# Performance work log

Measured on AMD Instinct MI355X. Metric: run time of the kernel, lower is better.

## Reference

```python
import jax, jax.numpy as jnp
import numpy as np

HEADS = 4
DIM_HEAD = 32
GROUPS = 32  # min(256//4, 32)
EPS = 1e-5


def setup_inputs() -> dict:
    key = jax.random.key(0)
    ks = jax.random.split(key, 6)
    B, C, H, W = 16, 256, 64, 64
    hidden = HEADS * DIM_HEAD  # 128
    return {
        "x": jax.random.normal(ks[0], (B, C, H, W), dtype=jnp.float32),
        "gn_w": jax.random.uniform(ks[1], (C,), dtype=jnp.float32),
        "gn_b": jax.random.normal(ks[2], (C,), dtype=jnp.float32) * 0.05,
        "qkv_w": jax.random.normal(ks[3], (3 * hidden, C), dtype=jnp.float32) * 0.05,
        "qkv_b": jax.random.normal(ks[4], (3 * hidden,), dtype=jnp.float32) * 0.05,
        "out_w": jax.random.normal(ks[5], (C, hidden), dtype=jnp.float32) * 0.05,
        "out_b": jnp.zeros((C,), dtype=jnp.float32),
    }


def _forward_single(x, gn_w, gn_b, qkv_w, qkv_b, out_w, out_b):
    # x: (c, h, w)
    c, h, w = x.shape
    # GroupNorm over (channels-in-group, h, w)
    xg = x.reshape(GROUPS, c // GROUPS, h, w)
    mean = xg.mean(axis=(1, 2, 3), keepdims=True)
    var = xg.var(axis=(1, 2, 3), keepdims=True)
    xn = ((xg - mean) * jax.lax.rsqrt(var + EPS)).reshape(c, h, w)
    xn = xn * gn_w[:, None, None] + gn_b[:, None, None]
    # 1x1 conv QKV projection
    qkv = jnp.einsum('oc,chw->ohw', qkv_w, xn) + qkv_b[:, None, None]
    qkv = qkv.reshape(3, HEADS, DIM_HEAD, h * w)
    q, k, v = qkv[0], qkv[1], qkv[2]
    k = jax.nn.softmax(k, axis=-1)  # softmax over spatial
    context = jnp.einsum('hdn,hen->hde', k, v)   # (heads, d, d)
    out = jnp.einsum('hde,hdn->hen', context, q)  # (heads, d, n)
    out = out.reshape(HEADS * DIM_HEAD, h, w)
    # 1x1 conv output projection
    return jnp.einsum('oc,chw->ohw', out_w, out) + out_b[:, None, None]


def reference(x, gn_w, gn_b, qkv_w, qkv_b, out_w, out_b):
    f = lambda xi: _forward_single(xi, gn_w, gn_b, qkv_w, qkv_b, out_w, out_b)
    return jax.vmap(f)(x)
```

## Files before the change

### kernel.cpp

```cpp
#include <hip/hip_runtime.h>
#include <stdint.h>

typedef unsigned short u16;
typedef __attribute__((ext_vector_type(8))) short bf16x8;
typedef __attribute__((ext_vector_type(4))) float f32x4;

#define B_   16
#define C_   256
#define HW_  4096
#define QR_  384
#define HID_ 128

__device__ __forceinline__ float b2f(u16 u) {
  union { uint32_t i; float f; } v; v.i = ((uint32_t)u) << 16; return v.f;
}
__device__ __forceinline__ u16 f2b(float f) {
  union { float f; uint32_t i; } v; v.f = f;
  uint32_t r = (v.i + 0x7FFFu + ((v.i >> 16) & 1u)) >> 16;
  return (u16)r;
}

__global__ __launch_bounds__(256) void gn_stats_conv_kernel(
    const float* __restrict__ x, const float* __restrict__ gnw,
    const float* __restrict__ gnb, float* __restrict__ scale,
    float* __restrict__ shiftv,
    const float* __restrict__ qkvw, u16* __restrict__ cqkvw)
{
  if (blockIdx.x >= 512) {
    int i = (blockIdx.x - 512) * 256 + threadIdx.x;
    float4 f = ((const float4*)qkvw)[i];
    ushort4 o;
    o.x = f2b(f.x); o.y = f2b(f.y); o.z = f2b(f.z); o.w = f2b(f.w);
    ((ushort4*)cqkvw)[i] = o;
    return;
  }
  int b = blockIdx.x >> 5, g = blockIdx.x & 31;
  const float* p = x + ((size_t)b * C_ + g * 8) * HW_;
  int t = threadIdx.x;
  float s = 0.f, sq = 0.f;
#pragma unroll
  for (int i = 0; i < 16; ++i) {
    float4 u0 = *(const float4*)(p + t * 8 + i * 2048);
    float4 u1 = *(const float4*)(p + t * 8 + i * 2048 + 4);
    s  += u0.x + u0.y + u0.z + u0.w + u1.x + u1.y + u1.z + u1.w;
    sq += u0.x*u0.x + u0.y*u0.y + u0.z*u0.z + u0.w*u0.w
        + u1.x*u1.x + u1.y*u1.y + u1.z*u1.z + u1.w*u1.w;
  }
#pragma unroll
  for (int off = 32; off > 0; off >>= 1) {
    s  += __shfl_down(s, off);
    sq += __shfl_down(sq, off);
  }
  __shared__ float ps[4], pq[4], mr[2];
  int lane = t & 63, w = t >> 6;
  if (lane == 0) { ps[w] = s; pq[w] = sq; }
  __syncthreads();
  if (t == 0) {
    float S = ps[0] + ps[1] + ps[2] + ps[3];
    float Q = pq[0] + pq[1] + pq[2] + pq[3];
    float mean = S * (1.f / 32768.f);
    float var  = Q * (1.f / 32768.f) - mean * mean;
    mr[0] = mean; mr[1] = rsqrtf(var + 1e-5f);
  }
  __syncthreads();
  if (t < 8) {
    int c = g * 8 + t;
    float sc = gnw[c] * mr[1];
    scale[b * C_ + c]  = sc;
    shiftv[b * C_ + c] = gnb[c] - mr[0] * sc;
  }
}

__global__ __launch_bounds__(256) void gn_transpose_kernel(
    const float* __restrict__ x, u16* __restrict__ dst,
    const float* __restrict__ scale, const float* __restrict__ shiftv)
{
  int nt = blockIdx.x, ct = blockIdx.y, b = blockIdx.z;
  const float* S = x + (size_t)b * C_ * HW_;
  u16* D = dst + (size_t)b * HW_ * C_;
  __shared__ __align__(16) u16 tile[64][136];
  int t = threadIdx.x;
  int n0 = nt * 128, c0 = ct * 64;
  int r = t >> 2, seg = (t & 3) * 32;
  float sc = scale[(size_t)b * C_ + c0 + r];
  float sh = shiftv[(size_t)b * C_ + c0 + r];
#pragma unroll
  for (int i = 0; i < 4; ++i) {
    const float* rp = S + (size_t)(c0 + r) * HW_ + n0 + seg + i * 8;
    float4 u0 = *(const float4*)(rp);
    float4 u1 = *(const float4*)(rp + 4);
    float f[8] = {u0.x, u0.y, u0.z, u0.w, u1.x, u1.y, u1.z, u1.w};
    uint4 o;
    uint32_t* op = (uint32_t*)&o;
#pragma unroll
    for (int j = 0; j < 4; ++j) {
      op[j] = (uint32_t)f2b(f[2 * j] * sc + sh)
            | ((uint32_t)f2b(f[2 * j + 1] * sc + sh) << 16);
    }
    *(uint4*)&tile[r][seg + i * 8] = o;
  }
  __syncthreads();
#pragma unroll
  for (int i = 0; i < 4; ++i) {
    int m = t * 4 + i;
    int n_l = m >> 3, cg = (m & 7) * 8;
    union { u16 v[8]; uint4 q; } pk;
#pragma unroll
    for (int e = 0; e < 8; ++e) pk.v[e] = tile[cg + e][n_l];
    *(uint4*)(D + (size_t)(n0 + n_l) * C_ + c0 + cg) = pk.q;
  }
}

__global__ __launch_bounds__(256) void qkv_gemm_kernel(
    const u16* __restrict__ A, const u16* __restrict__ Bt,
    const float* __restrict__ bias, u16* __restrict__ qkv,
    u16* __restrict__ q_t)
{
  const int K = C_;
  int nt = blockIdx.x, mt = blockIdx.y, b = blockIdx.z;
  const u16* Ab = A + (size_t)mt * 128 * K;
  const u16* Bb = Bt + (size_t)b * HW_ * C_ + (size_t)nt * 128 * K;
  __shared__ __align__(16) u16 smem[128 * 136];
  u16* lA = smem;
  u16* lB = smem + 8192;
  int t = threadIdx.x;
  int lane = t & 63, w = t >> 6;
  int quad = lane >> 4, l16 = lane & 15;
  int wm = (w >> 1) * 64, wn = (w & 1) * 64;
  f32x4 acc[4][4];
#pragma unroll
  for (int i = 0; i < 4; ++i)
#pragma unroll
    for (int j = 0; j < 4; ++j)
#pragma unroll
      for (int r = 0; r < 4; ++r) acc[i][j][r] = 0.f;

  for (int k0 = 0; k0 < K; k0 += 64) {
    __syncthreads();
#pragma unroll
    for (int q = 0; q < 4; ++q) {
      int ch = q * 256 + t;
      int row = ch >> 3, off = (ch & 7) * 8;
      __builtin_amdgcn_global_load_lds(
          (const __attribute__((address_space(1))) void*)(Ab + (size_t)row * K + k0 + off),
          (__attribute__((address_space(3))) void*)(lA + ch * 8), 16, 0, 0);
      __builtin_amdgcn_global_load_lds(
          (const __attribute__((address_space(1))) void*)(Bb + (size_t)row * K + k0 + off),
          (__attribute__((address_space(3))) void*)(lB + ch * 8), 16, 0, 0);
    }
    __syncthreads();
    const bf16x8* A8 = (const bf16x8*)lA;
    const bf16x8* B8 = (const bf16x8*)lB;
#pragma unroll
    for (int kk = 0; kk < 2; ++kk) {
      bf16x8 af[4], bfr[4];
#pragma unroll
      for (int i = 0; i < 4; ++i) af[i]  = A8[(wm + i * 16 + l16) * 8 + kk * 4 + quad];
#pragma unroll
      for (int j = 0; j < 4; ++j) bfr[j] = B8[(wn + j * 16 + l16) * 8 + kk * 4 + quad];
#pragma unroll
      for (int i = 0; i < 4; ++i)
#pragma unroll
        for (int j = 0; j < 4; ++j)
          acc[i][j] = __builtin_amdgcn_mfma_f32_16x16x32_bf16(af[i], bfr[j],
                                                              acc[i][j], 0, 0, 0);
    }
  }

  if (mt == 0) {
    __syncthreads();
#pragma unroll
    for (int i = 0; i < 4; ++i) {
      int o0 = wm + i * 16 + quad * 4;
      float b0 = bias[o0], b1 = bias[o0 + 1], b2 = bias[o0 + 2], b3 = bias[o0 + 3];
#pragma unroll
      for (int j = 0; j < 4; ++j) {
        int n_l = wn + j * 16 + l16;
        uint2 pk;
        pk.x = (uint32_t)f2b(acc[i][j][0] + b0) | ((uint32_t)f2b(acc[i][j][1] + b1) << 16);
        pk.y = (uint32_t)f2b(acc[i][j][2] + b2) | ((uint32_t)f2b(acc[i][j][3] + b3) << 16);
        *(uint2*)&smem[n_l * 136 + o0] = pk;
      }
    }
    __syncthreads();
    int n_l = t >> 1, half = t & 1;
    u16* dst = q_t + (size_t)b * HW_ * HID_ + (size_t)(nt * 128 + n_l) * HID_ + half * 64;
    const u16* srcp = smem + n_l * 136 + half * 64;
#pragma unroll
    for (int i = 0; i < 8; ++i)
      *(uint4*)(dst + i * 8) = *(const uint4*)(srcp + i * 8);
  } else {
#pragma unroll
    for (int i = 0; i < 4; ++i) {
#pragma unroll
      for (int rg = 0; rg < 4; ++rg) {
        int o = mt * 128 + wm + i * 16 + quad * 4 + rg;
        float bsv = bias[o];
        size_t rowbase = (size_t)b * QR_ * HW_ + (size_t)o * HW_;
#pragma unroll
        for (int j = 0; j < 4; ++j) {
          int n = nt * 128 + wn + j * 16 + l16;
          qkv[rowbase + n] = f2b(acc[i][j][rg] + bsv);
        }
      }
    }
  }
}

__global__ __launch_bounds__(1024) void ctxwf_kernel(
    const u16* __restrict__ qkv, const float* __restrict__ outw,
    u16* __restrict__ wf)
{
  int b = blockIdx.x >> 2, h = blockIdx.x & 3;
  const u16* kb = qkv + ((size_t)b * QR_ + 128 + h * 32) * HW_;
  const u16* vb = qkv + ((size_t)b * QR_ + 256 + h * 32) * HW_;
  int t = threadIdx.x;
  int w = t >> 6, lane = t & 63;
  int quad = lane >> 4, l16 = lane & 15;
  __shared__ float part[16][1024];
  __shared__ float cs[1024];
  __shared__ float2 sred[1024];
  __shared__ float sinv[32];
  f32x4 acc[2][2];
#pragma unroll
  for (int i = 0; i < 2; ++i)
#pragma unroll
    for (int j = 0; j < 2; ++j)
#pragma unroll
      for (int r = 0; r < 4; ++r) acc[i][j][r] = 0.f;
  float s0 = 0.f, s1 = 0.f;
  int kbase = w * 256;
  for (int it = 0; it < 8; ++it) {
    int n0 = kbase + it * 32 + quad * 8;
    bf16x8 k0 = *(const bf16x8*)(kb + (size_t)l16 * HW_ + n0);
    bf16x8 k1 = *(const bf16x8*)(kb + (size_t)(16 + l16) * HW_ + n0);
    bf16x8 v0 = *(const bf16x8*)(vb + (size_t)l16 * HW_ + n0);
    bf16x8 v1 = *(const bf16x8*)(vb + (size_t)(16 + l16) * HW_ + n0);
    bf16x8 a0, a1;
    const u16* k0p = (const u16*)&k0; u16* a0p = (u16*)&a0;
    const u16* k1p = (const u16*)&k1; u16* a1p = (u16*)&a1;
#pragma unroll
    for (int e = 0; e < 8; ++e) {
      float e0 = __expf(b2f(k0p[e]));
      float e1 = __expf(b2f(k1p[e]));
      s0 += e0; s1 += e1;
      a0p[e] = f2b(e0);
      a1p[e] = f2b(e1);
    }
    acc[0][0] = __builtin_amdgcn_mfma_f32_16x16x32_bf16(a0, v0, acc[0][0], 0, 0, 0);
    acc[0][1] = __builtin_amdgcn_mfma_f32_16x16x32_bf16(a0, v1, acc[0][1], 0, 0, 0);
    acc[1][0] = __builtin_amdgcn_mfma_f32_16x16x32_bf16(a1, v0, acc[1][0], 0, 0, 0);
    acc[1][1] = __builtin_amdgcn_mfma_f32_16x16x32_bf16(a1, v1, acc[1][1], 0, 0, 0);
  }
#pragma unroll
  for (int i = 0; i < 2; ++i)
#pragma unroll
    for (int j = 0; j < 2; ++j)
#pragma unroll
      for (int r = 0; r < 4; ++r) {
        int d = i * 16 + quad * 4 + r;
        int e = j * 16 + l16;
        part[w][d * 32 + e] = acc[i][j][r];
      }
  sred[t] = make_float2(s0, s1);
  __syncthreads();
  {
    float a = 0.f;
#pragma unroll
    for (int ww = 0; ww < 16; ++ww) a += part[ww][t];
    cs[t] = a;
  }
  if (t < 32) {
    int d = t, lsel = d & 15;
    float ssum = 0.f;
#pragma unroll
    for (int ww = 0; ww < 16; ++ww)
#pragma unroll
      for (int q = 0; q < 4; ++q) {
        float2 v2 = sred[ww * 64 + q * 16 + lsel];
        ssum += (d < 16) ? v2.x : v2.y;
      }
    sinv[d] = 1.f / ssum;
  }
  __syncthreads();

  int o = t & 255, dg = t >> 8;
  const float* wr = outw + (size_t)o * HID_ + h * 32;
  float wv[32];
#pragma unroll
  for (int e = 0; e < 32; ++e) wv[e] = wr[e];
  union { u16 v[8]; uint4 q; } pk;
#pragma unroll
  for (int dd = 0; dd < 8; ++dd) {
    int d = dg * 8 + dd;
    float a = 0.f;
#pragma unroll
    for (int e = 0; e < 32; ++e) a += wv[e] * cs[d * 32 + e];
    pk.v[dd] = f2b(a * sinv[d]);
  }
  *(uint4*)(wf + ((size_t)b * C_ + o) * HID_ + h * 32 + dg * 8) = pk.q;
}

__global__ __launch_bounds__(256) void out_gemm_kernel(
    const u16* __restrict__ A, const u16* __restrict__ Bt,
    const float* __restrict__ bias, float* __restrict__ Cout)
{
  const int K = HID_;
  int nt = blockIdx.x, mt = blockIdx.y, b = blockIdx.z;
  const u16* Ab = A + (size_t)b * C_ * HID_ + (size_t)mt * 128 * K;
  const u16* Bb = Bt + (size_t)b * HW_ * HID_ + (size_t)nt * 128 * K;
  __shared__ __align__(16) u16 lA[128 * 64];
  __shared__ __align__(16) u16 lB[128 * 64];
  int t = threadIdx.x;
  int lane = t & 63, w = t >> 6;
  int quad = lane >> 4, l16 = lane & 15;
  int wm = (w >> 1) * 64, wn = (w & 1) * 64;
  f32x4 acc[4][4];
#pragma unroll
  for (int i = 0; i < 4; ++i)
#pragma unroll
    for (int j = 0; j < 4; ++j)
#pragma unroll
      for (int r = 0; r < 4; ++r) acc[i][j][r] = 0.f;

  for (int k0 = 0; k0 < K; k0 += 64) {
    __syncthreads();
#pragma unroll
    for (int q = 0; q < 4; ++q) {
      int ch = q * 256 + t;
      int row = ch >> 3, off = (ch & 7) * 8;
      __builtin_amdgcn_global_load_lds(
          (const __attribute__((address_space(1))) void*)(Ab + (size_t)row * K + k0 + off),
          (__attribute__((address_space(3))) void*)(lA + ch * 8), 16, 0, 0);
      __builtin_amdgcn_global_load_lds(
          (const __attribute__((address_space(1))) void*)(Bb + (size_t)row * K + k0 + off),
          (__attribute__((address_space(3))) void*)(lB + ch * 8), 16, 0, 0);
    }
    __syncthreads();
    const bf16x8* A8 = (const bf16x8*)lA;
    const bf16x8* B8 = (const bf16x8*)lB;
#pragma unroll
    for (int kk = 0; kk < 2; ++kk) {
      bf16x8 af[4], bfr[4];
#pragma unroll
      for (int i = 0; i < 4; ++i) af[i]  = A8[(wm + i * 16 + l16) * 8 + kk * 4 + quad];
#pragma unroll
      for (int j = 0; j < 4; ++j) bfr[j] = B8[(wn + j * 16 + l16) * 8 + kk * 4 + quad];
#pragma unroll
      for (int i = 0; i < 4; ++i)
#pragma unroll
        for (int j = 0; j < 4; ++j)
          acc[i][j] = __builtin_amdgcn_mfma_f32_16x16x32_bf16(af[i], bfr[j],
                                                              acc[i][j], 0, 0, 0);
    }
  }
#pragma unroll
  for (int i = 0; i < 4; ++i) {
#pragma unroll
    for (int rg = 0; rg < 4; ++rg) {
      int o = mt * 128 + wm + i * 16 + quad * 4 + rg;
      float bsv = bias[o];
      size_t rowbase = (size_t)b * C_ * HW_ + (size_t)o * HW_;
#pragma unroll
      for (int j = 0; j < 4; ++j) {
        int n = nt * 128 + wn + j * 16 + l16;
        Cout[rowbase + n] = acc[i][j][rg] + bsv;
      }
    }
  }
}

extern "C" void kernel_launch(void* const* d_in, const int* in_sizes, int n_in,
                              void* d_out, int out_size, void* d_ws, size_t ws_size,
                              hipStream_t stream)
{
  const float* x    = (const float*)d_in[0];
  const float* gnw  = (const float*)d_in[1];
  const float* gnb  = (const float*)d_in[2];
  const float* qkvw = (const float*)d_in[3];
  const float* qkvb = (const float*)d_in[4];
  const float* outw = (const float*)d_in[5];
  const float* outb = (const float*)d_in[6];

  char* p = (char*)d_ws;
  float* scale  = (float*)p;            p += (size_t)B_ * C_ * 4;
  float* shiftv = (float*)p;            p += (size_t)B_ * C_ * 4;
  u16* cqkvw = (u16*)p;                 p += (size_t)QR_ * C_ * 2;
  u16* xn_t  = (u16*)p;                 p += (size_t)B_ * HW_ * C_ * 2;
  u16* qkv   = (u16*)p;                 p += (size_t)B_ * QR_ * HW_ * 2;
  u16* q_t   = (u16*)p;                 p += (size_t)B_ * HW_ * HID_ * 2;
  u16* wf    = (u16*)p;

  gn_stats_conv_kernel<<<608, 256, 0, stream>>>(x, gnw, gnb, scale, shiftv,
                                                qkvw, cqkvw);
  gn_transpose_kernel<<<dim3(32, 4, 16), 256, 0, stream>>>(x, xn_t, scale, shiftv);
  qkv_gemm_kernel<<<dim3(32, 3, 16), 256, 0, stream>>>(cqkvw, xn_t, qkvb, qkv, q_t);
  ctxwf_kernel<<<64, 1024, 0, stream>>>(qkv, outw, wf);
  out_gemm_kernel<<<dim3(32, 2, 16), 256, 0, stream>>>(wf, q_t, outb, (float*)d_out);
}
```

Measured before the change: 205.8 us.

## Fuse all stages into one persistent kernel with grid barriers

Replaces the five-kernel pipeline with a single persistent kernel of 256 blocks of 512 threads. The stages (GroupNorm stats, normalize-transpose, QKV GEMM, context, output GEMM) are separated by software grid barriers built on atomics. The context reduction is spread over all blocks with atomicAdd into global buffers, replacing the old 64-block kernel. The folded output weight is recomputed per tile inside the output GEMM. This removes launch gaps and the under-parallelised ctx stage, at the cost of spin-barrier overhead, a co-residency requirement for all 256 blocks, and redundant per-tile weight folding.

After: 449.4 us. +118.3%, slower.

```diff
diff --git a/kernel.cpp b/kernel.cpp
--- a/kernel.cpp
+++ b/kernel.cpp
@@ -8,8 +8,8 @@
 #define B_   16
 #define C_   256
 #define HW_  4096
-#define QR_  384
 #define HID_ 128
+#define NBLK 256
 
 __device__ __forceinline__ float b2f(u16 u) {
   union { uint32_t i; float f; } v; v.i = ((uint32_t)u) << 16; return v.f;
@@ -20,351 +20,397 @@
   return (u16)r;
 }
 
-__global__ __launch_bounds__(256) void gn_stats_conv_kernel(
+__global__ void init_kernel(unsigned* bar) {
+  if (threadIdx.x < 8) bar[threadIdx.x] = 0u;
+}
+
+__device__ __forceinline__ void grid_barrier(unsigned* bar) {
+  __syncthreads();
+  if (threadIdx.x == 0) {
+    __threadfence();
+    unsigned g = __hip_atomic_load(&bar[1], __ATOMIC_RELAXED, __HIP_MEMORY_SCOPE_AGENT);
+    unsigned a = __hip_atomic_fetch_add(&bar[0], 1u, __ATOMIC_ACQ_REL, __HIP_MEMORY_SCOPE_AGENT);
+    if (a == NBLK - 1) {
+      __hip_atomic_store(&bar[0], 0u, __ATOMIC_RELAXED, __HIP_MEMORY_SCOPE_AGENT);
+      __hip_atomic_store(&bar[1], g + 1u, __ATOMIC_RELEASE, __HIP_MEMORY_SCOPE_AGENT);
+    } else {
+      while (__hip_atomic_load(&bar[1], __ATOMIC_ACQUIRE, __HIP_MEMORY_SCOPE_AGENT) == g) {
+        __builtin_amdgcn_s_sleep(1);
+      }
+    }
+  }
+  __syncthreads();
+}
+
+__global__ __launch_bounds__(512, 2) void mega_kernel(
     const float* __restrict__ x, const float* __restrict__ gnw,
-    const float* __restrict__ gnb, float* __restrict__ scale,
-    float* __restrict__ shiftv,
-    const float* __restrict__ qkvw, u16* __restrict__ cqkvw)
+    const float* __restrict__ gnb, const float* __restrict__ qkvw,
+    const float* __restrict__ qkvb, const float* __restrict__ outw,
+    const float* __restrict__ outb, float* __restrict__ out,
+    unsigned* bar, float* scale, float* shiftv, u16* cqkvw,
+    u16* xn_t, u16* kv, u16* q_t, float* ctxg, float* sbuf)
 {
-  if (blockIdx.x >= 512) {
-    int i = (blockIdx.x - 512) * 256 + threadIdx.x;
-    float4 f = ((const float4*)qkvw)[i];
-    ushort4 o;
-    o.x = f2b(f.x); o.y = f2b(f.y); o.z = f2b(f.z); o.w = f2b(f.w);
-    ((ushort4*)cqkvw)[i] = o;
-    return;
-  }
-  int b = blockIdx.x >> 5, g = blockIdx.x & 31;
-  const float* p = x + ((size_t)b * C_ + g * 8) * HW_;
+  __shared__ __align__(16) char smem_raw[119296];
   int t = threadIdx.x;
-  float s = 0.f, sq = 0.f;
-#pragma unroll
-  for (int i = 0; i < 16; ++i) {
-    float4 u0 = *(const float4*)(p + t * 8 + i * 2048);
-    float4 u1 = *(const float4*)(p + t * 8 + i * 2048 + 4);
-    s  += u0.x + u0.y + u0.z + u0.w + u1.x + u1.y + u1.z + u1.w;
-    sq += u0.x*u0.x + u0.y*u0.y + u0.z*u0.z + u0.w*u0.w
-        + u1.x*u1.x + u1.y*u1.y + u1.z*u1.z + u1.w*u1.w;
-  }
-#pragma unroll
-  for (int off = 32; off > 0; off >>= 1) {
-    s  += __shfl_down(s, off);
-    sq += __shfl_down(sq, off);
-  }
-  __shared__ float ps[4], pq[4], mr[2];
-  int lane = t & 63, w = t >> 6;
-  if (lane == 0) { ps[w] = s; pq[w] = sq; }
-  __syncthreads();
-  if (t == 0) {
-    float S = ps[0] + ps[1] + ps[2] + ps[3];
-    float Q = pq[0] + pq[1] + pq[2] + pq[3];
-    float mean = S * (1.f / 32768.f);
-    float var  = Q * (1.f / 32768.f) - mean * mean;
-    mr[0] = mean; mr[1] = rsqrtf(var + 1e-5f);
-  }
-  __syncthreads();
-  if (t < 8) {
-    int c = g * 8 + t;
-    float sc = gnw[c] * mr[1];
-    scale[b * C_ + c]  = sc;
-    shiftv[b * C_ + c] = gnb[c] - mr[0] * sc;
-  }
-}
-
-__global__ __launch_bounds__(256) void gn_transpose_kernel(
-    const float* __restrict__ x, u16* __restrict__ dst,
-    const float* __restrict__ scale, const float* __restrict__ shiftv)
-{
-  int nt = blockIdx.x, ct = blockIdx.y, b = blockIdx.z;
-  const float* S = x + (size_t)b * C_ * HW_;
-  u16* D = dst + (size_t)b * HW_ * C_;
-  __shared__ __align__(16) u16 tile[64][136];
-  int t = threadIdx.x;
-  int n0 = nt * 128, c0 = ct * 64;
-  int r = t >> 2, seg = (t & 3) * 32;
-  float sc = scale[(size_t)b * C_ + c0 + r];
-  float sh = shiftv[(size_t)b * C_ + c0 + r];
-#pragma unroll
-  for (int i = 0; i < 4; ++i) {
-    const float* rp = S + (size_t)(c0 + r) * HW_ + n0 + seg + i * 8;
-    float4 u0 = *(const float4*)(rp);
-    float4 u1 = *(const float4*)(rp + 4);
-    float f[8] = {u0.x, u0.y, u0.z, u0.w, u1.x, u1.y, u1.z, u1.w};
-    uint4 o;
-    uint32_t* op = (uint32_t*)&o;
-#pragma unroll
-    for (int j = 0; j < 4; ++j) {
-      op[j] = (uint32_t)f2b(f[2 * j] * sc + sh)
-            | ((uint32_t)f2b(f[2 * j + 1] * sc + sh) << 16);
-    }
-    *(uint4*)&tile[r][seg + i * 8] = o;
-  }
-  __syncthreads();
-#pragma unroll
-  for (int i = 0; i < 4; ++i) {
-    int m = t * 4 + i;
-    int n_l = m >> 3, cg = (m & 7) * 8;
-    union { u16 v[8]; uint4 q; } pk;
-#pragma unroll
-    for (int e = 0; e < 8; ++e) pk.v[e] = tile[cg + e][n_l];
-    *(uint4*)(D + (size_t)(n0 + n_l) * C_ + c0 + cg) = pk.q;
-  }
-}
-
-__global__ __launch_bounds__(256) void qkv_gemm_kernel(
-    const u16* __restrict__ A, const u16* __restrict__ Bt,
-    const float* __restrict__ bias, u16* __restrict__ qkv,
-    u16* __restrict__ q_t)
-{
-  const int K = C_;
-  int nt = blockIdx.x, mt = blockIdx.y, b = blockIdx.z;
-  const u16* Ab = A + (size_t)mt * 128 * K;
-  const u16* Bb = Bt + (size_t)b * HW_ * C_ + (size_t)nt * 128 * K;
-  __shared__ __align__(16) u16 smem[128 * 136];
-  u16* lA = smem;
-  u16* lB = smem + 8192;
-  int t = threadIdx.x;
-  int lane = t & 63, w = t >> 6;
-  int quad = lane >> 4, l16 = lane & 15;
-  int wm = (w >> 1) * 64, wn = (w & 1) * 64;
-  f32x4 acc[4][4];
-#pragma unroll
-  for (int i = 0; i < 4; ++i)
-#pragma unroll
-    for (int j = 0; j < 4; ++j)
-#pragma unroll
-      for (int r = 0; r < 4; ++r) acc[i][j][r] = 0.f;
-
-  for (int k0 = 0; k0 < K; k0 += 64) {
+  int blk = blockIdx.x;
+
+  {
+    int gid = blk * 512 + t;
+    if (gid < 24576) {
+      float4 f = ((const float4*)qkvw)[gid];
+      ushort4 o;
+      o.x = f2b(f.x); o.y = f2b(f.y); o.z = f2b(f.z); o.w = f2b(f.w);
+      ((ushort4*)cqkvw)[gid] = o;
+    } else if (gid < 24576 + 16896) {
+      ((float4*)ctxg)[gid - 24576] = make_float4(0.f, 0.f, 0.f, 0.f);
+    }
+    int half = t >> 8, tid = t & 255;
+    int grp = blk * 2 + half;
+    int b = grp >> 5, g = grp & 31;
+    const float* p = x + ((size_t)b * C_ + g * 8) * HW_;
+    float s = 0.f, sq = 0.f;
+#pragma unroll
+    for (int i = 0; i < 16; ++i) {
+      float4 u0 = *(const float4*)(p + tid * 8 + i * 2048);
+      float4 u1 = *(const float4*)(p + tid * 8 + i * 2048 + 4);
+      s  += u0.x + u0.y + u0.z + u0.w + u1.x + u1.y + u1.z + u1.w;
+      sq += u0.x*u0.x + u0.y*u0.y + u0.z*u0.z + u0.w*u0.w
+          + u1.x*u1.x + u1.y*u1.y + u1.z*u1.z + u1.w*u1.w;
+    }
+#pragma unroll
+    for (int off = 32; off > 0; off >>= 1) {
+      s  += __shfl_down(s, off);
+      sq += __shfl_down(sq, off);
+    }
+    float* ps = (float*)smem_raw;
+    float* pq = ps + 8;
+    float* mrA = pq + 8;
+    int lane = t & 63, w = t >> 6;
+    if (lane == 0) { ps[w] = s; pq[w] = sq; }
     __syncthreads();
-#pragma unroll
-    for (int q = 0; q < 4; ++q) {
-      int ch = q * 256 + t;
-      int row = ch >> 3, off = (ch & 7) * 8;
-      __builtin_amdgcn_global_load_lds(
-          (const __attribute__((address_space(1))) void*)(Ab + (size_t)row * K + k0 + off),
-          (__attribute__((address_space(3))) void*)(lA + ch * 8), 16, 0, 0);
-      __builtin_amdgcn_global_load_lds(
-          (const __attribute__((address_space(1))) void*)(Bb + (size_t)row * K + k0 + off),
-          (__attribute__((address_space(3))) void*)(lB + ch * 8), 16, 0, 0);
+    if (tid == 0) {
+      float S = ps[half*4] + ps[half*4+1] + ps[half*4+2] + ps[half*4+3];
+      float Q = pq[half*4] + pq[half*4+1] + pq[half*4+2] + pq[half*4+3];
+      float mean = S * (1.f / 32768.f);
+      float var  = Q * (1.f / 32768.f) - mean * mean;
+      mrA[half*2]   = mean;
+      mrA[half*2+1] = rsqrtf(var + 1e-5f);
     }
     __syncthreads();
-    const bf16x8* A8 = (const bf16x8*)lA;
-    const bf16x8* B8 = (const bf16x8*)lB;
-#pragma unroll
-    for (int kk = 0; kk < 2; ++kk) {
-      bf16x8 af[4], bfr[4];
-#pragma unroll
-      for (int i = 0; i < 4; ++i) af[i]  = A8[(wm + i * 16 + l16) * 8 + kk * 4 + quad];
-#pragma unroll
-      for (int j = 0; j < 4; ++j) bfr[j] = B8[(wn + j * 16 + l16) * 8 + kk * 4 + quad];
+    if (tid < 8) {
+      int c = g * 8 + tid;
+      float sc = gnw[c] * mrA[half*2+1];
+      scale[b * C_ + c]  = sc;
+      shiftv[b * C_ + c] = gnb[c] - mrA[half*2] * sc;
+    }
+  }
+  grid_barrier(bar);
+
+  {
+    int sg = t >> 8, tid = t & 255;
+#pragma unroll 1
+    for (int iter = 0; iter < 4; ++iter) {
+      int task = iter * 512 + blk * 2 + sg;
+      int nt = task & 31, ct = (task >> 5) & 3, b = task >> 7;
+      const float* S = x + (size_t)b * C_ * HW_;
+      u16* D = xn_t + (size_t)b * HW_ * C_;
+      u16* tl = (u16*)smem_raw + sg * 8704;
+      int n0 = nt * 128, c0 = ct * 64;
+      int r = tid >> 2, seg = (tid & 3) * 32;
+      float sc = scale[(size_t)b * C_ + c0 + r];
+      float sh = shiftv[(size_t)b * C_ + c0 + r];
+#pragma unroll
+      for (int i = 0; i < 4; ++i) {
+        const float* rp = S + (size_t)(c0 + r) * HW_ + n0 + seg + i * 8;
+        float4 u0 = *(const float4*)(rp);
+        float4 u1 = *(const float4*)(rp + 4);
+        float f[8] = {u0.x, u0.y, u0.z, u0.w, u1.x, u1.y, u1.z, u1.w};
+        uint4 o;
+        uint32_t* op = (uint32_t*)&o;
+#pragma unroll
+        for (int j = 0; j < 4; ++j)
+          op[j] = (uint32_t)f2b(f[2*j] * sc + sh)
+                | ((uint32_t)f2b(f[2*j+1] * sc + sh) << 16);
+        *(uint4*)&tl[r * 136 + seg + i * 8] = o;
+      }
+      __syncthreads();
+#pragma unroll
+      for (int i = 0; i < 4; ++i) {
+        int m = tid * 4 + i;
+        int n_l = m >> 3, cg = (m & 7) * 8;
+        union { u16 v[8]; uint4 q; } pk;
+#pragma unroll
+        for (int e = 0; e < 8; ++e) pk.v[e] = tl[(cg + e) * 136 + n_l];
+        *(uint4*)(D + (size_t)(n0 + n_l) * C_ + c0 + cg) = pk.q;
+      }
+      __syncthreads();
+    }
+  }
+  grid_barrier(bar);
+
+  {
+    u16* lA = (u16*)smem_raw;
+    u16* lB = lA + 8192;
+    int lane = t & 63, w = t >> 6;
+    int quad = lane >> 4, l16 = lane & 15;
+    int wm = (w >> 2) * 64, wn = (w & 3) * 64;
+#pragma unroll 1
+    for (int iter = 0; iter < 3; ++iter) {
+      int task = iter * 256 + blk;
+      int b = task / 48, r48 = task % 48;
+      int mt = r48 >> 4, nt = r48 & 15;
+      const u16* Ab = cqkvw + (size_t)mt * 128 * 256;
+      const u16* Bb = xn_t + (size_t)b * HW_ * C_ + (size_t)nt * 256 * 256;
+      f32x4 acc[4][4];
 #pragma unroll
       for (int i = 0; i < 4; ++i)
 #pragma unroll
         for (int j = 0; j < 4; ++j)
-          acc[i][j] = __builtin_amdgcn_mfma_f32_16x16x32_bf16(af[i], bfr[j],
-                                                              acc[i][j], 0, 0, 0);
-    }
-  }
-
-  if (mt == 0) {
+#pragma unroll
+          for (int r = 0; r < 4; ++r) acc[i][j][r] = 0.f;
+      for (int k0 = 0; k0 < 256; k0 += 64) {
+        __syncthreads();
+#pragma unroll
+        for (int q = 0; q < 6; ++q) {
+          int ch = q * 512 + t;
+          if (ch < 1024) {
+            int row = ch >> 3, off = (ch & 7) * 8;
+            __builtin_amdgcn_global_load_lds(
+                (const __attribute__((address_space(1))) void*)(Ab + (size_t)row * 256 + k0 + off),
+                (__attribute__((address_space(3))) void*)(lA + ch * 8), 16, 0, 0);
+          } else {
+            int c2 = ch - 1024;
+            int row = c2 >> 3, off = (c2 & 7) * 8;
+            __builtin_amdgcn_global_load_lds(
+                (const __attribute__((address_space(1))) void*)(Bb + (size_t)row * 256 + k0 + off),
+                (__attribute__((address_space(3))) void*)(lB + c2 * 8), 16, 0, 0);
+          }
+        }
+        __syncthreads();
+        const bf16x8* A8 = (const bf16x8*)lA;
+        const bf16x8* B8 = (const bf16x8*)lB;
+#pragma unroll
+        for (int kk = 0; kk < 2; ++kk) {
+          bf16x8 af[4], bfr[4];
+#pragma unroll
+          for (int i = 0; i < 4; ++i) af[i]  = A8[(wm + i * 16 + l16) * 8 + kk * 4 + quad];
+#pragma unroll
+          for (int j = 0; j < 4; ++j) bfr[j] = B8[(wn + j * 16 + l16) * 8 + kk * 4 + quad];
+#pragma unroll
+          for (int i = 0; i < 4; ++i)
+#pragma unroll
+            for (int j = 0; j < 4; ++j)
+              acc[i][j] = __builtin_amdgcn_mfma_f32_16x16x32_bf16(af[i], bfr[j],
+                                                                  acc[i][j], 0, 0, 0);
+        }
+      }
+      __syncthreads();
+      if (mt == 0) {
+        u16* ot = (u16*)smem_raw;
+#pragma unroll
+        for (int i = 0; i < 4; ++i) {
+          int o0 = wm + i * 16 + quad * 4;
+          float b0 = qkvb[o0], b1 = qkvb[o0+1], b2 = qkvb[o0+2], b3 = qkvb[o0+3];
+#pragma unroll
+          for (int j = 0; j < 4; ++j) {
+            int n_l = wn + j * 16 + l16;
+            uint2 pk;
+            pk.x = (uint32_t)f2b(acc[i][j][0] + b0) | ((uint32_t)f2b(acc[i][j][1] + b1) << 16);
+            pk.y = (uint32_t)f2b(acc[i][j][2] + b2) | ((uint32_t)f2b(acc[i][j][3] + b3) << 16);
+            *(uint2*)&ot[n_l * 136 + o0] = pk;
+          }
+        }
+      } else {
+#pragma unroll
+        for (int i = 0; i < 4; ++i) {
+#pragma unroll
+          for (int rg = 0; rg < 4; ++rg) {
+            int o = mt * 128 + wm + i * 16 + quad * 4 + rg;
+            float bsv = qkvb[o];
+            u16* kr = kv + ((size_t)b * 256 + (o - 128)) * HW_;
+#pragma unroll
+            for (int j = 0; j < 4; ++j) {
+              int n = nt * 256 + wn + j * 16 + l16;
+              kr[n] = f2b(acc[i][j][rg] + bsv);
+            }
+          }
+        }
+      }
+      __syncthreads();
+      if (mt == 0) {
+        int n_l = t >> 1, half = t & 1;
+        u16* dst = q_t + (size_t)b * HW_ * HID_ + (size_t)(nt * 256 + n_l) * HID_ + half * 64;
+        const u16* sp = (const u16*)smem_raw + n_l * 136 + half * 64;
+#pragma unroll
+        for (int i = 0; i < 8; ++i)
+          *(uint4*)(dst + i * 8) = *(const uint4*)(sp + i * 8);
+      }
+    }
+  }
+  grid_barrier(bar);
+
+  {
+    int sg = t >> 8, tid = t & 255;
+    int task = blk * 2 + sg;
+    int b = task >> 5, h = (task >> 3) & 3, chunk = task & 7;
+    const u16* kb = kv + ((size_t)b * 256 + h * 32) * HW_;
+    const u16* vb = kv + ((size_t)b * 256 + 128 + h * 32) * HW_;
+    int wl = tid >> 6, lane = t & 63;
+    int quad = lane >> 4, l16 = lane & 15;
+    float* part = (float*)smem_raw + sg * 4608;
+    float* sred = part + 4096;
+    f32x4 acc[2][2];
+#pragma unroll
+    for (int i = 0; i < 2; ++i)
+#pragma unroll
+      for (int j = 0; j < 2; ++j)
+#pragma unroll
+        for (int r = 0; r < 4; ++r) acc[i][j][r] = 0.f;
+    float s0 = 0.f, s1 = 0.f;
+    int base = chunk * 512 + wl * 128;
+#pragma unroll 1
+    for (int it = 0; it < 4; ++it) {
+      int n0 = base + it * 32 + quad * 8;
+      bf16x8 k0 = *(const bf16x8*)(kb + (size_t)l16 * HW_ + n0);
+      bf16x8 k1 = *(const bf16x8*)(kb + (size_t)(16 + l16) * HW_ + n0);
+      bf16x8 v0 = *(const bf16x8*)(vb + (size_t)l16 * HW_ + n0);
+      bf16x8 v1 = *(const bf16x8*)(vb + (size_t)(16 + l16) * HW_ + n0);
+      bf16x8 a0, a1;
+      const u16* k0p = (const u16*)&k0; u16* a0p = (u16*)&a0;
+      const u16* k1p = (const u16*)&k1; u16* a1p = (u16*)&a1;
+#pragma unroll
+      for (int e = 0; e < 8; ++e) {
+        float e0 = __expf(b2f(k0p[e]));
+        float e1 = __expf(b2f(k1p[e]));
+        s0 += e0; s1 += e1;
+        a0p[e] = f2b(e0); a1p[e] = f2b(e1);
+      }
+      acc[0][0] = __builtin_amdgcn_mfma_f32_16x16x32_bf16(a0, v0, acc[0][0], 0, 0, 0);
+      acc[0][1] = __builtin_amdgcn_mfma_f32_16x16x32_bf16(a0, v1, acc[0][1], 0, 0, 0);
+      acc[1][0] = __builtin_amdgcn_mfma_f32_16x16x32_bf16(a1, v0, acc[1][0], 0, 0, 0);
+      acc[1][1] = __builtin_amdgcn_mfma_f32_16x16x32_bf16(a1, v1, acc[1][1], 0, 0, 0);
+    }
+#pragma unroll
+    for (int i = 0; i < 2; ++i)
+#pragma unroll
+      for (int j = 0; j < 2; ++j)
+#pragma unroll
+        for (int r = 0; r < 4; ++r) {
+          int d = i * 16 + quad * 4 + r;
+          int e = j * 16 + l16;
+          part[wl * 1024 + d * 32 + e] = acc[i][j][r];
+        }
+    sred[wl * 128 + (lane & 63) * 2]     = s0;
+    sred[wl * 128 + (lane & 63) * 2 + 1] = s1;
     __syncthreads();
+    float* cb = ctxg + (size_t)(b * 4 + h) * 1024;
 #pragma unroll
     for (int i = 0; i < 4; ++i) {
-      int o0 = wm + i * 16 + quad * 4;
-      float b0 = bias[o0], b1 = bias[o0 + 1], b2 = bias[o0 + 2], b3 = bias[o0 + 3];
-#pragma unroll
-      for (int j = 0; j < 4; ++j) {
-        int n_l = wn + j * 16 + l16;
-        uint2 pk;
-        pk.x = (uint32_t)f2b(acc[i][j][0] + b0) | ((uint32_t)f2b(acc[i][j][1] + b1) << 16);
-        pk.y = (uint32_t)f2b(acc[i][j][2] + b2) | ((uint32_t)f2b(acc[i][j][3] + b3) << 16);
-        *(uint2*)&smem[n_l * 136 + o0] = pk;
-      }
-    }
-    __syncthreads();
-    int n_l = t >> 1, half = t & 1;
-    u16* dst = q_t + (size_t)b * HW_ * HID_ + (size_t)(nt * 128 + n_l) * HID_ + half * 64;
-    const u16* srcp = smem + n_l * 136 + half * 64;
-#pragma unroll
-    for (int i = 0; i < 8; ++i)
-      *(uint4*)(dst + i * 8) = *(const uint4*)(srcp + i * 8);
-  } else {
-#pragma unroll
-    for (int i = 0; i < 4; ++i) {
-#pragma unroll
-      for (int rg = 0; rg < 4; ++rg) {
-        int o = mt * 128 + wm + i * 16 + quad * 4 + rg;
-        float bsv = bias[o];
-        size_t rowbase = (size_t)b * QR_ * HW_ + (size_t)o * HW_;
-#pragma unroll
-        for (int j = 0; j < 4; ++j) {
-          int n = nt * 128 + wn + j * 16 + l16;
-          qkv[rowbase + n] = f2b(acc[i][j][rg] + bsv);
-        }
-      }
-    }
-  }
-}
-
-__global__ __launch_bounds__(1024) void ctxwf_kernel(
-    const u16* __restrict__ qkv, const float* __restrict__ outw,
-    u16* __restrict__ wf)
-{
-  int b = blockIdx.x >> 2, h = blockIdx.x & 3;
-  const u16* kb = qkv + ((size_t)b * QR_ + 128 + h * 32) * HW_;
-  const u16* vb = qkv + ((size_t)b * QR_ + 256 + h * 32) * HW_;
-  int t = threadIdx.x;
-  int w = t >> 6, lane = t & 63;
-  int quad = lane >> 4, l16 = lane & 15;
-  __shared__ float part[16][1024];
-  __shared__ float cs[1024];
-  __shared__ float2 sred[1024];
-  __shared__ float sinv[32];
-  f32x4 acc[2][2];
-#pragma unroll
-  for (int i = 0; i < 2; ++i)
-#pragma unroll
-    for (int j = 0; j < 2; ++j)
-#pragma unroll
-      for (int r = 0; r < 4; ++r) acc[i][j][r] = 0.f;
-  float s0 = 0.f, s1 = 0.f;
-  int kbase = w * 256;
-  for (int it = 0; it < 8; ++it) {
-    int n0 = kbase + it * 32 + quad * 8;
-    bf16x8 k0 = *(const bf16x8*)(kb + (size_t)l16 * HW_ + n0);
-    bf16x8 k1 = *(const bf16x8*)(kb + (size_t)(16 + l16) * HW_ + n0);
-    bf16x8 v0 = *(const bf16x8*)(vb + (size_t)l16 * HW_ + n0);
-    bf16x8 v1 = *(const bf16x8*)(vb + (size_t)(16 + l16) * HW_ + n0);
-    bf16x8 a0, a1;
-    const u16* k0p = (const u16*)&k0; u16* a0p = (u16*)&a0;
-    const u16* k1p = (const u16*)&k1; u16* a1p = (u16*)&a1;
-#pragma unroll
-    for (int e = 0; e < 8; ++e) {
-      float e0 = __expf(b2f(k0p[e]));
-      float e1 = __expf(b2f(k1p[e]));
-      s0 += e0; s1 += e1;
-      a0p[e] = f2b(e0);
-      a1p[e] = f2b(e1);
-    }
-    acc[0][0] = __builtin_amdgcn_mfma_f32_16x16x32_bf16(a0, v0, acc[0][0], 0, 0, 0);
-    acc[0][1] = __builtin_amdgcn_mfma_f32_16x16x32_bf16(a0, v1, acc[0][1], 0, 0, 0);
-    acc[1][0] = __builtin_amdgcn_mfma_f32_16x16x32_bf16(a1, v0, acc[1][0], 0, 0, 0);
-    acc[1][1] = __builtin_amdgcn_mfma_f32_16x16x32_bf16(a1, v1, acc[1][1], 0, 0, 0);
-  }
-#pragma unroll
-  for (int i = 0; i < 2; ++i)
-#pragma unroll
-    for (int j = 0; j < 2; ++j)
-#pragma unroll
-      for (int r = 0; r < 4; ++r) {
-        int d = i * 16 + quad * 4 + r;
-        int e = j * 16 + l16;
-        part[w][d * 32 + e] = acc[i][j][r];
-      }
-  sred[t] = make_float2(s0, s1);
-  __syncthreads();
+      int idx = tid + i * 256;
+      atomicAdd(&cb[idx], part[idx] + part[1024 + idx] + part[2048 + idx] + part[3072 + idx]);
+    }
+    if (tid < 32) {
+      int d = tid;
+      float ss = 0.f;
+#pragma unroll
+      for (int w2 = 0; w2 < 4; ++w2)
+#pragma unroll
+        for (int q = 0; q < 4; ++q)
+          ss += sred[w2 * 128 + (q * 16 + (d & 15)) * 2 + (d >> 4)];
+      atomicAdd(&sbuf[(b * 4 + h) * 32 + d], ss);
+    }
+  }
+  grid_barrier(bar);
+
   {
-    float a = 0.f;
-#pragma unroll
-    for (int ww = 0; ww < 16; ++ww) a += part[ww][t];
-    cs[t] = a;
-  }
-  if (t < 32) {
-    int d = t, lsel = d & 15;
-    float ssum = 0.f;
-#pragma unroll
-    for (int ww = 0; ww < 16; ++ww)
+    u16* wfA = (u16*)smem_raw;
+    u16* lB  = (u16*)smem_raw + 256 * 136;
+    float* ctxs = (float*)(smem_raw + 69632 + 32768);
+    float* sinv = (float*)(smem_raw + 69632 + 32768 + 16384);
+    int lane = t & 63, w = t >> 6;
+    int quad = lane >> 4, l16 = lane & 15;
+    int wm = (w >> 1) * 64, wn = (w & 1) * 64;
+#pragma unroll 1
+    for (int iter = 0; iter < 2; ++iter) {
+      int task = iter * 256 + blk;
+      int nt = task & 31, b = task >> 5;
+      __syncthreads();
+      {
+        const float* cb = ctxg + (size_t)b * 4096;
+#pragma unroll
+        for (int i = 0; i < 8; ++i) ctxs[t + i * 512] = cb[t + i * 512];
+        if (t < 128) sinv[t] = 1.f / sbuf[b * 128 + t];
+      }
 #pragma unroll
       for (int q = 0; q < 4; ++q) {
-        float2 v2 = sred[ww * 64 + q * 16 + lsel];
-        ssum += (d < 16) ? v2.x : v2.y;
-      }
-    sinv[d] = 1.f / ssum;
-  }
-  __syncthreads();
-
-  int o = t & 255, dg = t >> 8;
-  const float* wr = outw + (size_t)o * HID_ + h * 32;
-  float wv[32];
-#pragma unroll
-  for (int e = 0; e < 32; ++e) wv[e] = wr[e];
-  union { u16 v[8]; uint4 q; } pk;
-#pragma unroll
-  for (int dd = 0; dd < 8; ++dd) {
-    int d = dg * 8 + dd;
-    float a = 0.f;
-#pragma unroll
-    for (int e = 0; e < 32; ++e) a += wv[e] * cs[d * 32 + e];
-    pk.v[dd] = f2b(a * sinv[d]);
-  }
-  *(uint4*)(wf + ((size_t)b * C_ + o) * HID_ + h * 32 + dg * 8) = pk.q;
-}
-
-__global__ __launch_bounds__(256) void out_gemm_kernel(
-    const u16* __restrict__ A, const u16* __restrict__ Bt,
-    const float* __restrict__ bias, float* __restrict__ Cout)
-{
-  const int K = HID_;
-  int nt = blockIdx.x, mt = blockIdx.y, b = blockIdx.z;
-  const u16* Ab = A + (size_t)b * C_ * HID_ + (size_t)mt * 128 * K;
-  const u16* Bb = Bt + (size_t)b * HW_ * HID_ + (size_t)nt * 128 * K;
-  __shared__ __align__(16) u16 lA[128 * 64];
-  __shared__ __align__(16) u16 lB[128 * 64];
-  int t = threadIdx.x;
-  int lane = t & 63, w = t >> 6;
-  int quad = lane >> 4, l16 = lane & 15;
-  int wm = (w >> 1) * 64, wn = (w & 1) * 64;
-  f32x4 acc[4][4];
-#pragma unroll
-  for (int i = 0; i < 4; ++i)
-#pragma unroll
-    for (int j = 0; j < 4; ++j)
-#pragma unroll
-      for (int r = 0; r < 4; ++r) acc[i][j][r] = 0.f;
-
-  for (int k0 = 0; k0 < K; k0 += 64) {
-    __syncthreads();
-#pragma unroll
-    for (int q = 0; q < 4; ++q) {
-      int ch = q * 256 + t;
-      int row = ch >> 3, off = (ch & 7) * 8;
-      __builtin_amdgcn_global_load_lds(
-          (const __attribute__((address_space(1))) void*)(Ab + (size_t)row * K + k0 + off),
-          (__attribute__((address_space(3))) void*)(lA + ch * 8), 16, 0, 0);
-      __builtin_amdgcn_global_load_lds(
-          (const __attribute__((address_space(1))) void*)(Bb + (size_t)row * K + k0 + off),
-          (__attribute__((address_space(3))) void*)(lB + ch * 8), 16, 0, 0);
-    }
-    __syncthreads();
-    const bf16x8* A8 = (const bf16x8*)lA;
-    const bf16x8* B8 = (const bf16x8*)lB;
-#pragma unroll
-    for (int kk = 0; kk < 2; ++kk) {
-      bf16x8 af[4], bfr[4];
-#pragma unroll
-      for (int i = 0; i < 4; ++i) af[i]  = A8[(wm + i * 16 + l16) * 8 + kk * 4 + quad];
-#pragma unroll
-      for (int j = 0; j < 4; ++j) bfr[j] = B8[(wn + j * 16 + l16) * 8 + kk * 4 + quad];
+        int ch = q * 512 + t;
+        int row = ch >> 4, off = (ch & 15) * 8;
+        __builtin_amdgcn_global_load_lds(
+            (const __attribute__((address_space(1))) void*)(q_t + ((size_t)b * HW_ + nt * 128 + row) * HID_ + off),
+            (__attribute__((address_space(3))) void*)(lB + ch * 8), 16, 0, 0);
+      }
+      __syncthreads();
+      {
+        int o = t >> 1, half = t & 1;
+        const float* wr = outw + (size_t)o * HID_ + half * 64;
+        float wv[64];
+#pragma unroll
+        for (int e = 0; e < 64; ++e) wv[e] = wr[e];
+        u16* dr = wfA + o * 136 + half * 64;
+#pragma unroll
+        for (int hh = 0; hh < 2; ++hh) {
+          int h = half * 2 + hh;
+#pragma unroll
+          for (int d = 0; d < 32; d += 2) {
+            float a0 = 0.f, a1 = 0.f;
+#pragma unroll
+            for (int e = 0; e < 32; ++e) {
+              a0 += wv[hh * 32 + e] * ctxs[h * 1024 + d * 32 + e];
+              a1 += wv[hh * 32 + e] * ctxs[h * 1024 + (d + 1) * 32 + e];
+            }
+            a0 *= sinv[half * 64 + hh * 32 + d];
+            a1 *= sinv[half * 64 + hh * 32 + d + 1];
+            *(uint32_t*)&dr[hh * 32 + d] = (uint32_t)f2b(a0) | ((uint32_t)f2b(a1) << 16);
+          }
+        }
+      }
+      __syncthreads();
+      f32x4 acc[4][4];
 #pragma unroll
       for (int i = 0; i < 4; ++i)
 #pragma unroll
         for (int j = 0; j < 4; ++j)
-          acc[i][j] = __builtin_amdgcn_mfma_f32_16x16x32_bf16(af[i], bfr[j],
-                                                              acc[i][j], 0, 0, 0);
-    }
-  }
-#pragma unroll
-  for (int i = 0; i < 4; ++i) {
-#pragma unroll
-    for (int rg = 0; rg < 4; ++rg) {
-      int o = mt * 128 + wm + i * 16 + quad * 4 + rg;
-      float bsv = bias[o];
-      size_t rowbase = (size_t)b * C_ * HW_ + (size_t)o * HW_;
-#pragma unroll
-      for (int j = 0; j < 4; ++j) {
-        int n = nt * 128 + wn + j * 16 + l16;
-        Cout[rowbase + n] = acc[i][j][rg] + bsv;
+#pragma unroll
+          for (int r = 0; r < 4; ++r) acc[i][j][r] = 0.f;
+      const bf16x8* A8 = (const bf16x8*)wfA;
+      const bf16x8* B8 = (const bf16x8*)lB;
+#pragma unroll
+      for (int kk = 0; kk < 4; ++kk) {
+        bf16x8 af[4], bfr[4];
+#pragma unroll
+        for (int i = 0; i < 4; ++i) af[i]  = A8[(wm + i * 16 + l16) * 17 + kk * 4 + quad];
+#pragma unroll
+        for (int j = 0; j < 4; ++j) bfr[j] = B8[(wn + j * 16 + l16) * 16 + kk * 4 + quad];
+#pragma unroll
+        for (int i = 0; i < 4; ++i)
+#pragma unroll
+          for (int j = 0; j < 4; ++j)
+            acc[i][j] = __builtin_amdgcn_mfma_f32_16x16x32_bf16(af[i], bfr[j],
+                                                                acc[i][j], 0, 0, 0);
+      }
+#pragma unroll
+      for (int i = 0; i < 4; ++i) {
+#pragma unroll
+        for (int rg = 0; rg < 4; ++rg) {
+          int o = wm + i * 16 + quad * 4 + rg;
+          float bsv = outb[o];
+          size_t rowb = ((size_t)b * C_ + o) * HW_;
+#pragma unroll
+          for (int j = 0; j < 4; ++j) {
+            int n = nt * 128 + wn + j * 16 + l16;
+            out[rowb + n] = acc[i][j][rg] + bsv;
+          }
+        }
       }
     }
   }
@@ -381,20 +427,21 @@
   const float* qkvb = (const float*)d_in[4];
   const float* outw = (const float*)d_in[5];
   const float* outb = (const float*)d_in[6];
+  float* out = (float*)d_out;
 
   char* p = (char*)d_ws;
+  unsigned* bar = (unsigned*)p;         p += 128;
   float* scale  = (float*)p;            p += (size_t)B_ * C_ * 4;
   float* shiftv = (float*)p;            p += (size_t)B_ * C_ * 4;
-  u16* cqkvw = (u16*)p;                 p += (size_t)QR_ * C_ * 2;
+  u16* cqkvw = (u16*)p;                 p += (size_t)384 * C_ * 2;
+  float* ctxg = (float*)p;              p += (size_t)B_ * 4 * 1024 * 4;
+  float* sbuf = (float*)p;              p += (size_t)B_ * 4 * 32 * 4;
   u16* xn_t  = (u16*)p;                 p += (size_t)B_ * HW_ * C_ * 2;
-  u16* qkv   = (u16*)p;                 p += (size_t)B_ * QR_ * HW_ * 2;
-  u16* q_t   = (u16*)p;                 p += (size_t)B_ * HW_ * HID_ * 2;
-  u16* wf    = (u16*)p;
-
-  gn_stats_conv_kernel<<<608, 256, 0, stream>>>(x, gnw, gnb, scale, shiftv,
-                                                qkvw, cqkvw);
-  gn_transpose_kernel<<<dim3(32, 4, 16), 256, 0, stream>>>(x, xn_t, scale, shiftv);
-  qkv_gemm_kernel<<<dim3(32, 3, 16), 256, 0, stream>>>(cqkvw, xn_t, qkvb, qkv, q_t);
-  ctxwf_kernel<<<64, 1024, 0, stream>>>(qkv, outw, wf);
-  out_gemm_kernel<<<dim3(32, 2, 16), 256, 0, stream>>>(wf, q_t, outb, (float*)d_out);
-}
+  u16* kv    = (u16*)p;                 p += (size_t)B_ * 256 * HW_ * 2;
+  u16* q_t   = (u16*)p;
+
+  init_kernel<<<1, 64, 0, stream>>>(bar);
+  mega_kernel<<<NBLK, 512, 0, stream>>>(x, gnw, gnb, qkvw, qkvb, outw, outb, out,
+                                        bar, scale, shiftv, cqkvw, xn_t, kv, q_t,
+                                        ctxg, sbuf);
+}
```
